# Kernel tuning notes

Hardware: AMD Instinct MI355X
Metric: run time of the kernel (lower is better)

## Reference

```python
import jax, jax.numpy as jnp
import numpy as np

V_TEXT = 256
V_TOTAL = 4352
B, H, TQ, TK = 8, 4, 800, 128
T_TOK = 1024
BLANK_LOGPROB = -8.0
NEG = -1e9  # finite stand-in for -inf (keeps grads nan-free)
CE_W = 1.5
ATTN_W = 10.0
ATTN_START = 5000


def setup_inputs() -> dict:
    key = jax.random.key(0)
    ks = jax.random.split(key, 6)
    logits = jax.random.normal(ks[0], (B, T_TOK, V_TOTAL), dtype=jnp.float32)
    attn_logprob = jax.random.normal(ks[1], (B, H, TQ, TK), dtype=jnp.float32)
    token_targets = jax.random.randint(ks[2], (B, T_TOK), V_TEXT, V_TOTAL, dtype=jnp.int32)
    audio_target_lens = jax.random.randint(ks[3], (B,), 512, T_TOK + 1, dtype=jnp.int32)
    src_lens = jax.random.randint(ks[4], (B,), 64, TK + 1, dtype=jnp.int32)  # key (text) lens
    out_lens = jax.random.randint(ks[5], (B,), 400, TQ + 1, dtype=jnp.int32)  # query (audio) lens
    return {"logits": logits, "attn_logprob": attn_logprob, "token_targets": token_targets,
            "audio_target_lens": audio_target_lens, "src_lens": src_lens, "out_lens": out_lens,
            "current_step": 6000}


def _masked_ce(logits, targets, valid_mask):
    # CE over the audio slice of the shared vocab; pads ignored; divide by mask count.
    v_audio = logits.shape[-1] - V_TEXT
    logp = jax.nn.log_softmax(logits[:, :, V_TEXT:], axis=-1)  # (B,T,Va)
    tgt = targets - V_TEXT
    valid = valid_mask & (targets != -100)
    safe = jnp.clip(tgt, 0, v_audio - 1)
    nll = -jnp.take_along_axis(logp, safe[..., None], axis=-1)[..., 0]  # (B,T)
    loss_sum = jnp.sum(jnp.where(valid, nll, 0.0))
    denom = jnp.maximum(jnp.sum(valid_mask), 1).astype(logp.dtype)
    return loss_sum / denom


def _forward_sum(attn_logprob, key_lens, query_lens):
    # Batched CTC forward-sum over all (batch, head) pairs.
    # Targets for item b are 1..K_b (all distinct), blank = class 0 (padded logit -8).
    Bb, Hh, Tq, Tk = attn_logprob.shape
    N = Bb * Hh
    lp = jnp.pad(attn_logprob, ((0, 0), (0, 0), (0, 0), (1, 0)), constant_values=BLANK_LOGPROB)
    lp = lp.reshape(N, Tq, Tk + 1)
    klens = jnp.repeat(key_lens, Hh)    # (N,)
    qlens = jnp.repeat(query_lens, Hh)  # (N,)
    # masked log_softmax over the first K_b+1 classes only (matches per-item slice)
    cls_valid = jnp.arange(Tk + 1)[None, None, :] < (klens[:, None, None] + 1)
    logp = jax.nn.log_softmax(jnp.where(cls_valid, lp, NEG), axis=-1)  # (N,Tq,Tk+1)

    S = 2 * Tk + 1
    s = jnp.arange(S)
    ext_label = jnp.where(s % 2 == 1, (s + 1) // 2, 0)       # blank,1,blank,2,...
    skip_ok = (s % 2 == 1) & (s >= 2)                        # labels distinct -> skip always ok
    ext_valid = s[None, :] < (2 * klens[:, None] + 1)        # (N,S)
    emit = logp[:, :, ext_label]                             # (N,Tq,S)

    alpha0 = jnp.full((N, S), NEG, dtype=logp.dtype)
    alpha0 = alpha0.at[:, 0].set(emit[:, 0, 0]).at[:, 1].set(emit[:, 0, 1])
    alpha0 = jnp.where(ext_valid, alpha0, NEG)

    def step(alpha, emit_t):
        sh1 = jnp.pad(alpha, ((0, 0), (1, 0)), constant_values=NEG)[:, :-1]
        sh2 = jnp.pad(alpha, ((0, 0), (2, 0)), constant_values=NEG)[:, :-2]
        sh2 = jnp.where(skip_ok[None, :], sh2, NEG)
        a = jnp.logaddexp(jnp.logaddexp(alpha, sh1), sh2) + emit_t
        a = jnp.where(ext_valid, a, NEG)
        return a, a

    _, alphas = jax.lax.scan(step, alpha0, jnp.moveaxis(emit[:, 1:], 1, 0))  # (Tq-1,N,S)
    alphas = jnp.concatenate([alpha0[None], alphas], axis=0)                 # (Tq,N,S)

    alpha_T = alphas[qlens - 1, jnp.arange(N)]  # (N,S) alpha at t = query_len-1
    e1 = jnp.take_along_axis(alpha_T, (2 * klens - 1)[:, None], axis=1)[:, 0]
    e2 = jnp.take_along_axis(alpha_T, (2 * klens)[:, None], axis=1)[:, 0]
    nll = -jnp.logaddexp(e1, e2)
    loss = nll / klens.astype(logp.dtype)  # torch CTCLoss 'mean' divides by target len
    loss = jnp.where(jnp.isfinite(loss) & (loss < 1e8), loss, 0.0)  # zero_infinity
    return jnp.mean(loss)  # == sum_b/B then sum_h/H of the original loops


def _losses(logits, attn_logprob, token_targets, audio_target_lens, src_lens, out_lens, current_step):
    t_tok = token_targets.shape[1]
    valid = jnp.arange(t_tok)[None, :] < audio_target_lens[:, None]
    token_loss = _masked_ce(logits, token_targets, valid)
    if current_step > ATTN_START:
        q = jnp.minimum(out_lens, attn_logprob.shape[2])
        k = jnp.minimum(src_lens, attn_logprob.shape[3])
        attn_loss = _forward_sum(attn_logprob, k, q)
    else:
        attn_loss = jnp.zeros((), dtype=logits.dtype)
    total = token_loss * CE_W + attn_loss * ATTN_W
    return jnp.stack([total, attn_loss, token_loss])


def reference(logits, attn_logprob, token_targets, audio_target_lens, src_lens, out_lens, current_step):
    return _losses(logits, attn_logprob, token_targets, audio_target_lens, src_lens, out_lens, current_step)
```

## Files before the change

kernel.cpp:

```cpp
#include <hip/hip_runtime.h>
#include <hip/hip_bf16.h>
#include <cstdint>
#include <cstddef>

#define V_TEXT   256
#define V_TOTAL  4352
#define V_AUDIO  4096
#define B_       8
#define H_       4
#define TQ_      800
#define TK_      128
#define T_TOK    1024
#define NSEQ     32
#define K2       1.4426950408889634f
#define LN2      0.6931471805599453f
#define EB8      11.541560327111707f
#define EM8      3.3546262790251185e-04f
#define FNEGINF  (-3.0e38f)
#define CHK      60
#define NCH      14

template <int CTRL>
__device__ __forceinline__ float dpp_mov(float x, float old) {
    return __int_as_float(__builtin_amdgcn_update_dpp(
        __float_as_int(old), __float_as_int(x), CTRL, 0xf, 0xf, false));
}
__device__ __forceinline__ float dpp_shr1_old(float x, float old) {
    return dpp_mov<0x138>(x, old);
}
__device__ __forceinline__ float lane_bcast(float x, int lane) {
    return __int_as_float(__builtin_amdgcn_readlane(__float_as_int(x), lane));
}
__device__ __forceinline__ float wave_max(float x) {
    x = fmaxf(x, dpp_mov<0x111>(x, FNEGINF));
    x = fmaxf(x, dpp_mov<0x112>(x, FNEGINF));
    x = fmaxf(x, dpp_mov<0x114>(x, FNEGINF));
    x = fmaxf(x, dpp_mov<0x118>(x, FNEGINF));
    x = fmaxf(x, dpp_mov<0x142>(x, FNEGINF));
    x = fmaxf(x, dpp_mov<0x143>(x, FNEGINF));
    return lane_bcast(x, 63);
}
__device__ __forceinline__ float wave_sum(float x) {
    x += dpp_mov<0x111>(x, 0.0f);
    x += dpp_mov<0x112>(x, 0.0f);
    x += dpp_mov<0x114>(x, 0.0f);
    x += dpp_mov<0x118>(x, 0.0f);
    x += dpp_mov<0x142>(x, 0.0f);
    x += dpp_mov<0x143>(x, 0.0f);
    return lane_bcast(x, 63);
}

__global__ __launch_bounds__(256) void ce_kernel(
    const float* __restrict__ logits, const int* __restrict__ targets,
    const int* __restrict__ alens, float* __restrict__ nll_out)
{
    int w = threadIdx.x >> 6, lane = threadIdx.x & 63;
    int row = blockIdx.x * 4 + w;
    const float* p = logits + (size_t)row * V_TOTAL + V_TEXT;

    float4 v0 = *reinterpret_cast<const float4*>(p + lane * 4);
    float4 v1 = *reinterpret_cast<const float4*>(p + lane * 4 + 1024);
    float4 v2 = *reinterpret_cast<const float4*>(p + lane * 4 + 2048);
    float4 v3 = *reinterpret_cast<const float4*>(p + lane * 4 + 3072);
    int tg = targets[row];

    float m = fmaxf(fmaxf(fmaxf(v0.x, v0.y), fmaxf(v0.z, v0.w)),
                    fmaxf(fmaxf(v1.x, v1.y), fmaxf(v1.z, v1.w)));
    m = fmaxf(m, fmaxf(fmaxf(v2.x, v2.y), fmaxf(v2.z, v2.w)));
    m = fmaxf(m, fmaxf(fmaxf(v3.x, v3.y), fmaxf(v3.z, v3.w)));
    m = wave_max(m);

    float mn = -m * K2;
    float s =
      __builtin_exp2f(__builtin_fmaf(v0.x,K2,mn)) + __builtin_exp2f(__builtin_fmaf(v0.y,K2,mn))
    + __builtin_exp2f(__builtin_fmaf(v0.z,K2,mn)) + __builtin_exp2f(__builtin_fmaf(v0.w,K2,mn))
    + __builtin_exp2f(__builtin_fmaf(v1.x,K2,mn)) + __builtin_exp2f(__builtin_fmaf(v1.y,K2,mn))
    + __builtin_exp2f(__builtin_fmaf(v1.z,K2,mn)) + __builtin_exp2f(__builtin_fmaf(v1.w,K2,mn))
    + __builtin_exp2f(__builtin_fmaf(v2.x,K2,mn)) + __builtin_exp2f(__builtin_fmaf(v2.y,K2,mn))
    + __builtin_exp2f(__builtin_fmaf(v2.z,K2,mn)) + __builtin_exp2f(__builtin_fmaf(v2.w,K2,mn))
    + __builtin_exp2f(__builtin_fmaf(v3.x,K2,mn)) + __builtin_exp2f(__builtin_fmaf(v3.y,K2,mn))
    + __builtin_exp2f(__builtin_fmaf(v3.z,K2,mn)) + __builtin_exp2f(__builtin_fmaf(v3.w,K2,mn));
    s = wave_sum(s);

    if (lane == 0) {
        float lse = m + __builtin_log2f(s) * LN2;
        int b = row >> 10, t = row & (T_TOK - 1);
        bool valid = (t < alens[b]) && (tg != -100);
        float nll = 0.0f;
        if (valid) {
            int idx = min(max(tg - V_TEXT, 0), V_AUDIO - 1);
            nll = lse - p[idx];
        }
        nll_out[row] = nll;
    }
}

__device__ __forceinline__ void stage_rows(
    float* db, const float* __restrict__ abase, int g0, int k, int q,
    int lane, float& prod, int& acc)
{
    int half = lane >> 5, col = (lane & 31) * 4;
    #pragma unroll 6
    for (int i = 0; i < CHK / 2; i++) {
        int r  = 2 * i + half;
        int rg = g0 + r;
        int rc = min(rg, TQ_ - 1);
        float4 v = *reinterpret_cast<const float4*>(abase + (size_t)rc * TK_ + col);
        float e0 = (col + 0 < k) ? __builtin_exp2f(v.x * K2) : 0.0f;
        float e1 = (col + 1 < k) ? __builtin_exp2f(v.y * K2) : 0.0f;
        float e2 = (col + 2 < k) ? __builtin_exp2f(v.z * K2) : 0.0f;
        float e3 = (col + 3 < k) ? __builtin_exp2f(v.w * K2) : 0.0f;
        *reinterpret_cast<float4*>(db + r * TK_ + col) = make_float4(e0, e1, e2, e3);

        float ps = (e0 + e1) + (e2 + e3);
        ps += dpp_mov<0x111>(ps, 0.0f);
        ps += dpp_mov<0x112>(ps, 0.0f);
        ps += dpp_mov<0x114>(ps, 0.0f);
        ps += dpp_mov<0x118>(ps, 0.0f);
        ps += dpp_mov<0x142>(ps, 0.0f);
        ps += EM8;
        prod *= (rg < q) ? ps : 1.0f;
        if ((i % 3) == 2) {
            int b = __float_as_int(prod);
            acc += (b >> 23) - 127;
            prod = __int_as_float((b & 0x007fffff) | 0x3f800000);
        }
    }
}

__global__ __launch_bounds__(128) void rec_kernel(
    const float* __restrict__ attn,
    const int* __restrict__ src_lens, const int* __restrict__ out_lens,
    float* __restrict__ loss_out)
{
    __shared__ float buf[2][CHK][TK_];
    __shared__ float csh;
    int n   = blockIdx.x;
    int tid = threadIdx.x;
    int wid = tid >> 6, lane = tid & 63;
    int k = min(src_lens[n >> 2], TK_);
    int q = min(out_lens[n >> 2], TQ_);
    int ncha = (q + CHK - 1) / CHK;
    const float* abase = attn + (size_t)n * TQ_ * TK_;

    float prod = 1.0f;
    int   acc  = 0;

    float p0 = (wid == 0 && lane == 0) ? 1.0f : 0.0f;
    float p1 = 0.0f, p2 = 0.0f, p3 = 0.0f, p4 = 0.0f, p3s = 0.0f;
    int   Mtot = 0;
    int   rsc  = 0;

    if (wid == 1) stage_rows(&buf[0][0][0], abase, 0, k, q, lane, prod, acc);
    __syncthreads();

#define SSTEP(xv)                                                            \
    do {                                                                     \
        float c01 = p0 + p3s;                   \
        float c12 = p2 + p1;                                                 \
        float n4  = (p4 + p3) * EM8;            \
        p0 = c01 * EM8;                         \
        p1 = (p1 + c01) * xv.x;             \
        p2 = c12 * EM8;                                                      \
        p3 = (p3 + c12) * xv.y;             \
        p4 = n4;                                                             \
        p3s = dpp_shr1_old(p3, 0.0f);      \
    } while (0)

#define RESCALE()                                                            \
    do {                                                                     \
        float wm = fmaxf(fmaxf(fmaxf(p0, p1), fmaxf(p2, p3)),                \
                         fmaxf(p4, p3s));                                    \
        wm = wave_max(wm);                                                   \
        int ebits = __float_as_int(wm) & 0x7f800000;                         \
        if (ebits > 0) {                      \
            int se = 294 - (ebits >> 23);              \
            se = se < 1 ? 1 : (se > 254 ? 254 : se);                         \
            float sc = __int_as_float(se << 23);                             \
            Mtot += 127 - se;                                                \
            p0 *= sc; p1 *= sc; p2 *= sc; p3 *= sc; p4 *= sc; p3s *= sc;     \
        }                                                                    \
    } while (0)

    for (int c = 0; c < ncha; c++) {
        if (wid == 1) {
            if (c + 1 < ncha)
                stage_rows(&buf[(c + 1) & 1][0][0], abase, (c + 1) * CHK,
                           k, q, lane, prod, acc);
        } else {
            const float* lb = &buf[c & 1][0][2 * lane];
            int lim = min(CHK, q - c * CHK);
            int ts = 0;
            if (ts < lim) {
#define LD(j) (*reinterpret_cast<const float2*>(lb + min((j), CHK - 1) * TK_))
                float2 A = LD(0), Bv = LD(1), Cv = LD(2), Dv = LD(3);
                for (; ts + 4 <= lim; ts += 4) {
                    float2 nA = LD(ts + 4), nB = LD(ts + 5),
                           nC = LD(ts + 6), nD = LD(ts + 7);
                    SSTEP(A); SSTEP(Bv); SSTEP(Cv); SSTEP(Dv);
                    if (++rsc == 2) { rsc = 0; RESCALE(); }
                    A = nA; Bv = nB; Cv = nC; Dv = nD;
                }
                for (; ts < lim; ts++) { SSTEP(A); A = Bv; Bv = Cv; Cv = Dv; }
#undef LD
            }
        }
        __syncthreads();
    }
#undef SSTEP
#undef RESCALE

    if (wid == 1) {
        float cl = __builtin_log2f(prod) + (float)acc;
        float cs = lane_bcast(cl, 31) + lane_bcast(cl, 63);
        if (lane == 0) csh = cs;
    }
    __syncthreads();

    if (wid == 0) {
        int s1 = 2 * k - 1, s2 = 2 * k;
        float e1v, e2v;
        {
            int l = s1 >> 2, r = s1 & 3;
            float c1 = __shfl(p1, l), c3 = __shfl(p3, l);
            e1v = (r == 1) ? c1 : c3;
        }
        if (s2 == 256) {
            e2v = __shfl(p4, 63);
        } else {
            int l = s2 >> 2, r = s2 & 3;
            float c0 = __shfl(p0, l), c2 = __shfl(p2, l);
            e2v = (r == 0) ? c0 : c2;
        }
        float l2 = __builtin_log2f(e1v + e2v) + (float)Mtot - csh;
        float nll = -l2 * LN2;
        float loss = nll / (float)k;
        if (!(isfinite(loss) && loss < 1.0e8f)) loss = 0.0f;
        if (lane == 0) loss_out[n] = loss;
    }
}

__global__ __launch_bounds__(256) void fin_kernel(
    const float* __restrict__ nll, const int* __restrict__ alens,
    const int* __restrict__ step, const float* __restrict__ attn_losses,
    float* __restrict__ out)
{
    __shared__ float red[4];
    int tid = threadIdx.x;
    float s = 0.0f;
    for (int i = tid; i < B_ * T_TOK; i += 256) s += nll[i];
    #pragma unroll
    for (int off = 32; off > 0; off >>= 1) s += __shfl_xor(s, off);
    if ((tid & 63) == 0) red[tid >> 6] = s;
    __syncthreads();
    if (tid == 0) {
        float ce_sum = red[0] + red[1] + red[2] + red[3];
        int denom = 0;
        for (int b = 0; b < B_; b++) denom += min(alens[b], T_TOK);
        denom = max(denom, 1);
        float token = ce_sum / (float)denom;
        float a = 0.0f;
        for (int i = 0; i < NSEQ; i++) a += attn_losses[i];
        a *= (1.0f / NSEQ);
        if (step[0] <= 5000) a = 0.0f;
        out[0] = 1.5f * token + 10.0f * a;
        out[1] = a;
        out[2] = token;
    }
}

extern "C" void kernel_launch(void* const* d_in, const int* in_sizes, int n_in,
                              void* d_out, int out_size, void* d_ws, size_t ws_size,
                              hipStream_t stream)
{
    const float* logits  = (const float*)d_in[0];
    const float* attn    = (const float*)d_in[1];
    const int*   targets = (const int*)d_in[2];
    const int*   alens   = (const int*)d_in[3];
    const int*   slens   = (const int*)d_in[4];
    const int*   olens   = (const int*)d_in[5];
    const int*   step    = (const int*)d_in[6];
    float* out = (float*)d_out;
    float* ws  = (float*)d_ws;

    float* ws_attn = ws;
    float* ws_nll  = ws + 64;

    ce_kernel <<<dim3(B_ * T_TOK / 4), dim3(256), 0, stream>>>(logits, targets, alens, ws_nll);
    rec_kernel<<<dim3(NSEQ),           dim3(128), 0, stream>>>(attn, slens, olens, ws_attn);
    fin_kernel<<<dim3(1),              dim3(256), 0, stream>>>(ws_nll, alens, step, ws_attn, out);
}
```

Before: 281.4 us.

## Fuse CE and forward-sum kernels, use three producer waves with smaller chunks

Merges the CE kernel and the CTC recurrence kernel into one launch. The 32 recurrence blocks come first, so the long serial forward-sum runs alongside the CE rows instead of after them. Within each recurrence block, three producer waves now stage 30-row chunks, each loading 5 rows up front, instead of one wave staging 60 rows. This shortens the producer's critical path per chunk, at the cost of more barriers. The rescale target exponent is also adjusted for the shorter interval between rescales.

```diff
diff --git a/kernel.cpp b/kernel.cpp
--- a/kernel.cpp
+++ b/kernel.cpp
@@ -17,8 +17,7 @@
 #define EB8      11.541560327111707f
 #define EM8      3.3546262790251185e-04f
 #define FNEGINF  (-3.0e38f)
-#define CHK      60
-#define NCH      14
+#define CHK      30
 
 template <int CTRL>
 __device__ __forceinline__ float dpp_mov(float x, float old) {
@@ -40,76 +39,27 @@
     x = fmaxf(x, dpp_mov<0x143>(x, FNEGINF));
     return lane_bcast(x, 63);
 }
-__device__ __forceinline__ float wave_sum(float x) {
-    x += dpp_mov<0x111>(x, 0.0f);
-    x += dpp_mov<0x112>(x, 0.0f);
-    x += dpp_mov<0x114>(x, 0.0f);
-    x += dpp_mov<0x118>(x, 0.0f);
-    x += dpp_mov<0x142>(x, 0.0f);
-    x += dpp_mov<0x143>(x, 0.0f);
-    return lane_bcast(x, 63);
-}
-
-__global__ __launch_bounds__(256) void ce_kernel(
-    const float* __restrict__ logits, const int* __restrict__ targets,
-    const int* __restrict__ alens, float* __restrict__ nll_out)
-{
-    int w = threadIdx.x >> 6, lane = threadIdx.x & 63;
-    int row = blockIdx.x * 4 + w;
-    const float* p = logits + (size_t)row * V_TOTAL + V_TEXT;
-
-    float4 v0 = *reinterpret_cast<const float4*>(p + lane * 4);
-    float4 v1 = *reinterpret_cast<const float4*>(p + lane * 4 + 1024);
-    float4 v2 = *reinterpret_cast<const float4*>(p + lane * 4 + 2048);
-    float4 v3 = *reinterpret_cast<const float4*>(p + lane * 4 + 3072);
-    int tg = targets[row];
-
-    float m = fmaxf(fmaxf(fmaxf(v0.x, v0.y), fmaxf(v0.z, v0.w)),
-                    fmaxf(fmaxf(v1.x, v1.y), fmaxf(v1.z, v1.w)));
-    m = fmaxf(m, fmaxf(fmaxf(v2.x, v2.y), fmaxf(v2.z, v2.w)));
-    m = fmaxf(m, fmaxf(fmaxf(v3.x, v3.y), fmaxf(v3.z, v3.w)));
-    m = wave_max(m);
-
-    float mn = -m * K2;
-    float s =
-      __builtin_exp2f(__builtin_fmaf(v0.x,K2,mn)) + __builtin_exp2f(__builtin_fmaf(v0.y,K2,mn))
-    + __builtin_exp2f(__builtin_fmaf(v0.z,K2,mn)) + __builtin_exp2f(__builtin_fmaf(v0.w,K2,mn))
-    + __builtin_exp2f(__builtin_fmaf(v1.x,K2,mn)) + __builtin_exp2f(__builtin_fmaf(v1.y,K2,mn))
-    + __builtin_exp2f(__builtin_fmaf(v1.z,K2,mn)) + __builtin_exp2f(__builtin_fmaf(v1.w,K2,mn))
-    + __builtin_exp2f(__builtin_fmaf(v2.x,K2,mn)) + __builtin_exp2f(__builtin_fmaf(v2.y,K2,mn))
-    + __builtin_exp2f(__builtin_fmaf(v2.z,K2,mn)) + __builtin_exp2f(__builtin_fmaf(v2.w,K2,mn))
-    + __builtin_exp2f(__builtin_fmaf(v3.x,K2,mn)) + __builtin_exp2f(__builtin_fmaf(v3.y,K2,mn))
-    + __builtin_exp2f(__builtin_fmaf(v3.z,K2,mn)) + __builtin_exp2f(__builtin_fmaf(v3.w,K2,mn));
-    s = wave_sum(s);
-
-    if (lane == 0) {
-        float lse = m + __builtin_log2f(s) * LN2;
-        int b = row >> 10, t = row & (T_TOK - 1);
-        bool valid = (t < alens[b]) && (tg != -100);
-        float nll = 0.0f;
-        if (valid) {
-            int idx = min(max(tg - V_TEXT, 0), V_AUDIO - 1);
-            nll = lse - p[idx];
-        }
-        nll_out[row] = nll;
-    }
-}
-
-__device__ __forceinline__ void stage_rows(
-    float* db, const float* __restrict__ abase, int g0, int k, int q,
+
+__device__ __forceinline__ void stage_rows3(
+    float* db, const float* __restrict__ abase, int g0, int pw, int k, int q,
     int lane, float& prod, int& acc)
 {
     int half = lane >> 5, col = (lane & 31) * 4;
-    #pragma unroll 6
-    for (int i = 0; i < CHK / 2; i++) {
-        int r  = 2 * i + half;
+    int i0 = pw * 5;
+    float4 v[5];
+    #pragma unroll
+    for (int u = 0; u < 5; u++) {
+        int rc = min(g0 + 2 * (i0 + u) + half, TQ_ - 1);
+        v[u] = *reinterpret_cast<const float4*>(abase + (size_t)rc * TK_ + col);
+    }
+    #pragma unroll
+    for (int u = 0; u < 5; u++) {
+        int r  = 2 * (i0 + u) + half;
         int rg = g0 + r;
-        int rc = min(rg, TQ_ - 1);
-        float4 v = *reinterpret_cast<const float4*>(abase + (size_t)rc * TK_ + col);
-        float e0 = (col + 0 < k) ? __builtin_exp2f(v.x * K2) : 0.0f;
-        float e1 = (col + 1 < k) ? __builtin_exp2f(v.y * K2) : 0.0f;
-        float e2 = (col + 2 < k) ? __builtin_exp2f(v.z * K2) : 0.0f;
-        float e3 = (col + 3 < k) ? __builtin_exp2f(v.w * K2) : 0.0f;
+        float e0 = (col + 0 < k) ? __builtin_exp2f(v[u].x * K2) : 0.0f;
+        float e1 = (col + 1 < k) ? __builtin_exp2f(v[u].y * K2) : 0.0f;
+        float e2 = (col + 2 < k) ? __builtin_exp2f(v[u].z * K2) : 0.0f;
+        float e3 = (col + 3 < k) ? __builtin_exp2f(v[u].w * K2) : 0.0f;
         *reinterpret_cast<float4*>(db + r * TK_ + col) = make_float4(e0, e1, e2, e3);
 
         float ps = (e0 + e1) + (e2 + e3);
@@ -120,7 +70,7 @@
         ps += dpp_mov<0x142>(ps, 0.0f);
         ps += EM8;
         prod *= (rg < q) ? ps : 1.0f;
-        if ((i % 3) == 2) {
+        if (u & 1) {
             int b = __float_as_int(prod);
             acc += (b >> 23) - 127;
             prod = __int_as_float((b & 0x007fffff) | 0x3f800000);
@@ -128,18 +78,69 @@
     }
 }
 
-__global__ __launch_bounds__(128) void rec_kernel(
-    const float* __restrict__ attn,
-    const int* __restrict__ src_lens, const int* __restrict__ out_lens,
-    float* __restrict__ loss_out)
+__global__ __launch_bounds__(256) void fused_kernel(
+    const float* __restrict__ logits, const int* __restrict__ targets,
+    const int* __restrict__ alens,
+    const float* __restrict__ attn, const int* __restrict__ slens,
+    const int* __restrict__ olens,
+    float* __restrict__ nll_out, float* __restrict__ loss_out)
 {
     __shared__ float buf[2][CHK][TK_];
-    __shared__ float csh;
-    int n   = blockIdx.x;
+    __shared__ float cshp[4];
+
     int tid = threadIdx.x;
     int wid = tid >> 6, lane = tid & 63;
-    int k = min(src_lens[n >> 2], TK_);
-    int q = min(out_lens[n >> 2], TQ_);
+
+    if (blockIdx.x >= NSEQ) {
+        int row = (blockIdx.x - NSEQ) * 4 + wid;
+        const float* p = logits + (size_t)row * V_TOTAL + V_TEXT;
+
+        float4 v0 = *reinterpret_cast<const float4*>(p + lane * 4);
+        float4 v1 = *reinterpret_cast<const float4*>(p + lane * 4 + 1024);
+        float4 v2 = *reinterpret_cast<const float4*>(p + lane * 4 + 2048);
+        float4 v3 = *reinterpret_cast<const float4*>(p + lane * 4 + 3072);
+        int tg = targets[row];
+
+        float m = fmaxf(fmaxf(fmaxf(v0.x, v0.y), fmaxf(v0.z, v0.w)),
+                        fmaxf(fmaxf(v1.x, v1.y), fmaxf(v1.z, v1.w)));
+        m = fmaxf(m, fmaxf(fmaxf(v2.x, v2.y), fmaxf(v2.z, v2.w)));
+        m = fmaxf(m, fmaxf(fmaxf(v3.x, v3.y), fmaxf(v3.z, v3.w)));
+        m = wave_max(m);
+
+        float mn = -m * K2;
+        float s =
+          __builtin_exp2f(__builtin_fmaf(v0.x,K2,mn)) + __builtin_exp2f(__builtin_fmaf(v0.y,K2,mn))
+        + __builtin_exp2f(__builtin_fmaf(v0.z,K2,mn)) + __builtin_exp2f(__builtin_fmaf(v0.w,K2,mn))
+        + __builtin_exp2f(__builtin_fmaf(v1.x,K2,mn)) + __builtin_exp2f(__builtin_fmaf(v1.y,K2,mn))
+        + __builtin_exp2f(__builtin_fmaf(v1.z,K2,mn)) + __builtin_exp2f(__builtin_fmaf(v1.w,K2,mn))
+        + __builtin_exp2f(__builtin_fmaf(v2.x,K2,mn)) + __builtin_exp2f(__builtin_fmaf(v2.y,K2,mn))
+        + __builtin_exp2f(__builtin_fmaf(v2.z,K2,mn)) + __builtin_exp2f(__builtin_fmaf(v2.w,K2,mn))
+        + __builtin_exp2f(__builtin_fmaf(v3.x,K2,mn)) + __builtin_exp2f(__builtin_fmaf(v3.y,K2,mn))
+        + __builtin_exp2f(__builtin_fmaf(v3.z,K2,mn)) + __builtin_exp2f(__builtin_fmaf(v3.w,K2,mn));
+        s += dpp_mov<0x111>(s, 0.0f);
+        s += dpp_mov<0x112>(s, 0.0f);
+        s += dpp_mov<0x114>(s, 0.0f);
+        s += dpp_mov<0x118>(s, 0.0f);
+        s += dpp_mov<0x142>(s, 0.0f);
+        s  = lane_bcast(s, 31) + lane_bcast(s, 63);
+
+        if (lane == 0) {
+            float lse = m + __builtin_log2f(s) * LN2;
+            int b = row >> 10, t = row & (T_TOK - 1);
+            bool valid = (t < alens[b]) && (tg != -100);
+            float nll = 0.0f;
+            if (valid) {
+                int idx = min(max(tg - V_TEXT, 0), V_AUDIO - 1);
+                nll = lse - p[idx];
+            }
+            nll_out[row] = nll;
+        }
+        return;
+    }
+
+    int n = blockIdx.x;
+    int k = min(slens[n >> 2], TK_);
+    int q = min(olens[n >> 2], TQ_);
     int ncha = (q + CHK - 1) / CHK;
     const float* abase = attn + (size_t)n * TQ_ * TK_;
 
@@ -151,20 +152,20 @@
     int   Mtot = 0;
     int   rsc  = 0;
 
-    if (wid == 1) stage_rows(&buf[0][0][0], abase, 0, k, q, lane, prod, acc);
+    if (wid > 0) stage_rows3(&buf[0][0][0], abase, 0, wid - 1, k, q, lane, prod, acc);
     __syncthreads();
 
 #define SSTEP(xv)                                                            \
     do {                                                                     \
-        float c01 = p0 + p3s;                   \
+        float c01 = p0 + p3s;                                                \
         float c12 = p2 + p1;                                                 \
-        float n4  = (p4 + p3) * EM8;            \
-        p0 = c01 * EM8;                         \
-        p1 = (p1 + c01) * xv.x;             \
+        float n4  = (p4 + p3) * EM8;                                         \
+        p0 = c01 * EM8;                                                      \
+        p1 = (p1 + c01) * xv.x;                                              \
         p2 = c12 * EM8;                                                      \
-        p3 = (p3 + c12) * xv.y;             \
+        p3 = (p3 + c12) * xv.y;                                              \
         p4 = n4;                                                             \
-        p3s = dpp_shr1_old(p3, 0.0f);      \
+        p3s = dpp_shr1_old(p3, 0.0f);                                        \
     } while (0)
 
 #define RESCALE()                                                            \
@@ -174,7 +175,7 @@
         wm = wave_max(wm);                                                   \
         int ebits = __float_as_int(wm) & 0x7f800000;                         \
         if (ebits > 0) {                      \
-            int se = 294 - (ebits >> 23);              \
+            int se = 274 - (ebits >> 23);              \
             se = se < 1 ? 1 : (se > 254 ? 254 : se);                         \
             float sc = __int_as_float(se << 23);                             \
             Mtot += 127 - se;                                                \
@@ -183,10 +184,10 @@
     } while (0)
 
     for (int c = 0; c < ncha; c++) {
-        if (wid == 1) {
+        if (wid > 0) {
             if (c + 1 < ncha)
-                stage_rows(&buf[(c + 1) & 1][0][0], abase, (c + 1) * CHK,
-                           k, q, lane, prod, acc);
+                stage_rows3(&buf[(c + 1) & 1][0][0], abase, (c + 1) * CHK,
+                            wid - 1, k, q, lane, prod, acc);
         } else {
             const float* lb = &buf[c & 1][0][2 * lane];
             int lim = min(CHK, q - c * CHK);
@@ -210,14 +211,15 @@
 #undef SSTEP
 #undef RESCALE
 
-    if (wid == 1) {
+    if (wid > 0) {
         float cl = __builtin_log2f(prod) + (float)acc;
         float cs = lane_bcast(cl, 31) + lane_bcast(cl, 63);
-        if (lane == 0) csh = cs;
+        if (lane == 0) cshp[wid] = cs;
     }
     __syncthreads();
 
     if (wid == 0) {
+        float csh = cshp[1] + cshp[2] + cshp[3];
         int s1 = 2 * k - 1, s2 = 2 * k;
         float e1v, e2v;
         {
@@ -286,7 +288,7 @@
     float* ws_attn = ws;
     float* ws_nll  = ws + 64;
 
-    ce_kernel <<<dim3(B_ * T_TOK / 4), dim3(256), 0, stream>>>(logits, targets, alens, ws_nll);
-    rec_kernel<<<dim3(NSEQ),           dim3(128), 0, stream>>>(attn, slens, olens, ws_attn);
-    fin_kernel<<<dim3(1),              dim3(256), 0, stream>>>(ws_nll, alens, step, ws_attn, out);
-}
+    fused_kernel<<<dim3(NSEQ + B_ * T_TOK / 4), dim3(256), 0, stream>>>(
+        logits, targets, alens, attn, slens, olens, ws_nll, ws_attn);
+    fin_kernel<<<dim3(1), dim3(256), 0, stream>>>(ws_nll, alens, step, ws_attn, out);
+}
```

Measured after the change: 238.0 us. -15.4%, faster.
